# Performance work log

Measured on AMD Instinct MI355X. Metric: run time of the kernel, lower is better.

## Reference

```python
import jax, jax.numpy as jnp
import numpy as np

B, T, W, F, H = 4, 1024, 33, 512, 8
DK = F // H


def setup_inputs() -> dict:
    key = jax.random.key(0)
    ks = jax.random.split(key, 12)
    s = 1.0 / np.sqrt(F)
    return {
        "query": jax.random.normal(ks[0], (B, T, F), jnp.float32),
        "key": jax.random.normal(ks[1], (B, T, W, F), jnp.float32),
        "value": jax.random.normal(ks[2], (B, T, W, F), jnp.float32),
        "mask": jnp.ones((B, 1, T, W), jnp.int32),
        "Wq": jax.random.uniform(ks[3], (F, F), jnp.float32, -s, s),
        "bq": jax.random.uniform(ks[4], (F,), jnp.float32, -s, s),
        "Wk": jax.random.uniform(ks[5], (F, F), jnp.float32, -s, s),
        "bk": jax.random.uniform(ks[6], (F,), jnp.float32, -s, s),
        "Wv": jax.random.uniform(ks[7], (F, F), jnp.float32, -s, s),
        "bv": jax.random.uniform(ks[8], (F,), jnp.float32, -s, s),
        "Wo": jax.random.uniform(ks[9], (F, F), jnp.float32, -s, s),
        "bo": jax.random.uniform(ks[10], (F,), jnp.float32, -s, s),
    }


def reference(query, key, value, mask, Wq, bq, Wk, bk, Wv, bv, Wo, bo):
    b, t, w, f = key.shape
    # projections
    q = (query @ Wq + bq).reshape(b, t, H, DK)            # (B,T,H,Dk)
    k = (key @ Wk + bk).reshape(b, t, w, H, DK)           # (B,T,W,H,Dk)
    v = (value @ Wv + bv).reshape(b, t, w, H, DK)
    # windowed scores: each query attends to its own window of keys
    scores = jnp.einsum("bthd,btwhd->bhtw", q, k) / jnp.sqrt(jnp.asarray(DK, q.dtype))
    m = (mask == 0)                                       # (B,1,T,W), broadcasts over heads
    min_value = jnp.finfo(scores.dtype).min
    scores = jnp.where(m, min_value, scores)
    attn = jax.nn.softmax(scores, axis=-1)
    attn = jnp.where(m, 0.0, attn)                        # (B,H,T,W)
    x = jnp.einsum("bhtw,btwhd->bthd", attn, v).reshape(b, t, H * DK)
    return x @ Wo + bo
```

## Files before the change

kernel.cpp:

```cpp
#include <hip/hip_runtime.h>
#include <hip/hip_bf16.h>
#include <cstdint>

#define B_ 4
#define T_ 1024
#define W_ 33
#define F_ 512
#define H_ 8
#define DK_ 64

typedef __attribute__((ext_vector_type(8))) short short8;
typedef __attribute__((ext_vector_type(4))) float f32x4;

__device__ __forceinline__ float b2f(ushort u) {
  return __uint_as_float(((uint32_t)u) << 16);
}
__device__ __forceinline__ ushort f2b(float f) {
  union { __hip_bfloat16 b; ushort u; } cv;
  cv.b = __float2bfloat16(f);
  return cv.u;
}

__global__ void convert_w(const float* __restrict__ Wq, const float* __restrict__ Wk,
                          const float* __restrict__ Wv, const float* __restrict__ Wo,
                          ushort* __restrict__ out)
{
  int which = blockIdx.y;
  const float* src = (which == 0) ? Wq : (which == 1) ? Wk : (which == 2) ? Wv : Wo;
  ushort* dst = out + (size_t)which * 262144;
  int idx = blockIdx.x * 256 + threadIdx.x;
  int e = idx & 7;
  int l = (idx >> 3) & 63;
  float v;
  if (which == 1) {
    int kc  = (idx >> 9) & 1;
    int ntf = (idx >> 10) & 31;
    int h   = idx >> 15;
    v = src[(size_t)(ntf * 16 + (l & 15)) * 512 + h * 64 + kc * 32 + ((l >> 4) << 3) + e];
  } else {
    int kc = (idx >> 9) & 15;
    int nt = idx >> 13;
    int k = kc * 32 + ((l >> 4) << 3) + e;
    int n = (nt << 4) + (l & 15);
    v = src[(size_t)k * 512 + n];
  }
  dst[idx] = f2b(v);
}

template<bool A_F32, bool OUT_F32>
__global__ __launch_bounds__(256, 2)
void gemm_pipe(const void* __restrict__ Ap, const ushort* __restrict__ Bf,
               const float* __restrict__ bias, void* __restrict__ Cp, float scale)
{
  __shared__ ushort lA[3][128 * 64];

  const int tid  = threadIdx.x;
  const int lane = tid & 63;
  const int wid  = tid >> 6;
  const int wr   = wid >> 1, wc = wid & 1;
  const int lrow = lane & 15;
  const int lk8  = (lane >> 4) * 8;

  int nwg  = gridDim.x;
  int xcd  = blockIdx.x & 7;
  int slot = blockIdx.x >> 3;
  int q8   = nwg >> 3, r8 = nwg & 7;
  int base = (xcd < r8) ? xcd * (q8 + 1) : r8 * (q8 + 1) + (xcd - r8) * q8;
  int L    = base + slot;
  int bm   = L >> 2;
  int bn   = L & 3;

  int lb_[4];
  size_t asrc_[4];
#pragma unroll
  for (int p = 0; p < 4; ++p) {
    int c   = p * 256 + tid;
    int row = c >> 3;
    int kc  = (c & 7) * 8;
    lb_[p]  = (row * 128 + kc * 2) ^ ((row & 7) << 4);
    asrc_[p] = (size_t)(bm * 128 + row) * 512 + kc;
  }

  const int ntb = bn * 8 + wc * 4;

  float4 P0a0[4], P0a1[4], P1a0[4], P1a1[4];
  short8 P0r[4], P1r[4];
  short8 Q0[8], Q1[8];

  auto issueA = [&](int ks, float4 (&d0)[4], float4 (&d1)[4], short8 (&dr)[4]) {
#pragma unroll
    for (int p = 0; p < 4; ++p) {
      if (A_F32) {
        const float* src = (const float*)Ap + asrc_[p] + ks * 64;
        d0[p] = *(const float4*)src;
        d1[p] = *(const float4*)(src + 4);
      } else {
        dr[p] = *(const short8*)((const ushort*)Ap + asrc_[p] + ks * 64);
      }
    }
  };
  auto lwriteA = [&](int buf, float4 (&d0)[4], float4 (&d1)[4], short8 (&dr)[4]) {
#pragma unroll
    for (int p = 0; p < 4; ++p) {
      short8 hv;
      if (A_F32) {
        hv[0] = (short)f2b(d0[p].x); hv[1] = (short)f2b(d0[p].y);
        hv[2] = (short)f2b(d0[p].z); hv[3] = (short)f2b(d0[p].w);
        hv[4] = (short)f2b(d1[p].x); hv[5] = (short)f2b(d1[p].y);
        hv[6] = (short)f2b(d1[p].z); hv[7] = (short)f2b(d1[p].w);
      } else {
        hv = dr[p];
      }
      *(short8*)((char*)lA[buf] + lb_[p]) = hv;
    }
  };
  auto loadB = [&](int ks, short8 (&dq)[8]) {
#pragma unroll
    for (int kk = 0; kk < 2; ++kk)
#pragma unroll
      for (int nf = 0; nf < 4; ++nf)
        dq[kk * 4 + nf] = *(const short8*)(Bf +
            (((size_t)(ntb + nf) * 16 + ks * 2 + kk) * 64 + lane) * 8);
  };

  f32x4 acc[4][4];
#pragma unroll
  for (int i = 0; i < 4; ++i)
#pragma unroll
    for (int j = 0; j < 4; ++j) acc[i][j] = {0.f, 0.f, 0.f, 0.f};

  auto computeStep = [&](int buf, short8 (&dq)[8]) {
#pragma unroll
    for (int kk = 0; kk < 2; ++kk) {
      short8 af[4];
#pragma unroll
      for (int mf = 0; mf < 4; ++mf) {
        int row = wr * 64 + mf * 16 + lrow;
        int off = (row * 128 + (kk * 32 + lk8) * 2) ^ ((row & 7) << 4);
        af[mf] = *(const short8*)((const char*)lA[buf] + off);
      }
#pragma unroll
      for (int mf = 0; mf < 4; ++mf)
#pragma unroll
        for (int nf = 0; nf < 4; ++nf)
          acc[mf][nf] = __builtin_amdgcn_mfma_f32_16x16x32_bf16(af[mf], dq[kk * 4 + nf], acc[mf][nf], 0, 0, 0);
    }
  };

  issueA(0, P0a0, P0a1, P0r);
  issueA(1, P1a0, P1a1, P1r);
  loadB(0, Q0);
  lwriteA(0, P0a0, P0a1, P0r);
  __syncthreads();

#define GSTEP(T, PWa0, PWa1, PWr, PIa0, PIa1, PIr, QW, QR)                    \
  {                                                                           \
    if ((T) + 1 < 8) lwriteA(((T) + 1) % 3, PWa0, PWa1, PWr);                 \
    if ((T) + 2 < 8) issueA((T) + 2, PIa0, PIa1, PIr);                        \
    if ((T) + 1 < 8) loadB((T) + 1, QW);                                      \
    computeStep((T) % 3, QR);                                                 \
    if ((T) < 7) __syncthreads();                                             \
  }

  GSTEP(0, P1a0, P1a1, P1r, P0a0, P0a1, P0r, Q1, Q0)
  GSTEP(1, P0a0, P0a1, P0r, P1a0, P1a1, P1r, Q0, Q1)
  GSTEP(2, P1a0, P1a1, P1r, P0a0, P0a1, P0r, Q1, Q0)
  GSTEP(3, P0a0, P0a1, P0r, P1a0, P1a1, P1r, Q0, Q1)
  GSTEP(4, P1a0, P1a1, P1r, P0a0, P0a1, P0r, Q1, Q0)
  GSTEP(5, P0a0, P0a1, P0r, P1a0, P1a1, P1r, Q0, Q1)
  GSTEP(6, P1a0, P1a1, P1r, P0a0, P0a1, P0r, Q1, Q0)
  GSTEP(7, P0a0, P0a1, P0r, P1a0, P1a1, P1r, Q0, Q1)
#undef GSTEP

  float bs[4];
#pragma unroll
  for (int nf = 0; nf < 4; ++nf)
    bs[nf] = bias[bn * 128 + wc * 64 + nf * 16 + lrow];

  const int r0 = (lane >> 4) * 4;
#pragma unroll
  for (int mf = 0; mf < 4; ++mf) {
#pragma unroll
    for (int nf = 0; nf < 4; ++nf) {
      int gcol = bn * 128 + wc * 64 + nf * 16 + lrow;
#pragma unroll
      for (int r = 0; r < 4; ++r) {
        int grow = bm * 128 + wr * 64 + mf * 16 + r0 + r;
        float val = (acc[mf][nf][r] + bs[nf]) * scale;
        if (OUT_F32) ((float*)Cp)[(size_t)grow * 512 + gcol] = val;
        else         ((ushort*)Cp)[(size_t)grow * 512 + gcol] = f2b(val);
      }
    }
  }
}

__global__ __launch_bounds__(256, 4)
void r_gemm(const ushort* __restrict__ q, const ushort* __restrict__ WkR,
            ushort* __restrict__ R)
{
  const int tid  = threadIdx.x;
  const int lane = tid & 63;
  const int wid  = tid >> 6;
  const int lr   = lane & 15;
  const int l8   = (lane >> 4) * 8;
  const int mg   = blockIdx.x >> 1;
  const int nh   = blockIdx.x & 1;
  const int h    = blockIdx.y;
  const int m0   = mg * 64;
  const int ntb  = nh * 16 + wid * 4;

  short8 af[2][4], bg[2][4];
#pragma unroll
  for (int ks = 0; ks < 2; ++ks)
#pragma unroll
    for (int mf = 0; mf < 4; ++mf)
      af[ks][mf] = *(const short8*)(q + (size_t)(m0 + mf * 16 + lr) * 512 + h * 64 + ks * 32 + l8);
#pragma unroll
  for (int ks = 0; ks < 2; ++ks)
#pragma unroll
    for (int nf = 0; nf < 4; ++nf)
      bg[ks][nf] = *(const short8*)(WkR + ((size_t)((h * 32 + ntb + nf) * 2 + ks) * 64 + lane) * 8);

  f32x4 acc[4][4];
#pragma unroll
  for (int i = 0; i < 4; ++i)
#pragma unroll
    for (int j = 0; j < 4; ++j) acc[i][j] = {0.f, 0.f, 0.f, 0.f};

#pragma unroll
  for (int ks = 0; ks < 2; ++ks)
#pragma unroll
    for (int mf = 0; mf < 4; ++mf)
#pragma unroll
      for (int nf = 0; nf < 4; ++nf)
        acc[mf][nf] = __builtin_amdgcn_mfma_f32_16x16x32_bf16(af[ks][mf], bg[ks][nf], acc[mf][nf], 0, 0, 0);

  const int rr = (lane >> 4) * 4;
#pragma unroll
  for (int mf = 0; mf < 4; ++mf)
#pragma unroll
    for (int nf = 0; nf < 4; ++nf) {
      int col = nh * 256 + wid * 64 + nf * 16 + lr;
#pragma unroll
      for (int r = 0; r < 4; ++r) {
        int row = m0 + mf * 16 + rr + r;
        R[((size_t)row * 8 + h) * 512 + col] = f2b(acc[mf][nf][r]);
      }
    }
}

__global__ __launch_bounds__(256, 4)
void attn_fused(const float* __restrict__ key, const float* __restrict__ value,
                const ushort* __restrict__ R, const int* __restrict__ mask,
                ushort* __restrict__ g, float* __restrict__ asum)
{
  __shared__ float la[W_][8];
  __shared__ float linv[8];

  const int tid  = threadIdx.x;
  const int lane = tid & 63;
  const int wv   = tid >> 6;
  const int bt   = blockIdx.x;

  int mreg = 0;
  if (lane < W_) mreg = mask[(size_t)bt * W_ + lane];
  unsigned long long mbits = __ballot(mreg != 0);

  const int h0 = wv * 2;
  float Rf[2][8];
  {
    const ushort* Rb = R + (size_t)bt * 4096 + lane * 8;
    short8 rv0 = *(const short8*)(Rb + (size_t)h0 * 512);
    short8 rv1 = *(const short8*)(Rb + (size_t)(h0 + 1) * 512);
#pragma unroll
    for (int j = 0; j < 8; ++j) {
      Rf[0][j] = b2f((ushort)rv0[j]);
      Rf[1][j] = b2f((ushort)rv1[j]);
    }
  }

  const float* kb = key + (size_t)bt * (W_ * 512) + lane * 8;
#pragma unroll 3
  for (int w = 0; w < W_; ++w) {
    float4 ka = *(const float4*)(kb + (size_t)w * 512);
    float4 kc = *(const float4*)(kb + (size_t)w * 512 + 4);
    float s0 = ka.x * Rf[0][0] + ka.y * Rf[0][1] + ka.z * Rf[0][2] + ka.w * Rf[0][3]
             + kc.x * Rf[0][4] + kc.y * Rf[0][5] + kc.z * Rf[0][6] + kc.w * Rf[0][7];
    float s1 = ka.x * Rf[1][0] + ka.y * Rf[1][1] + ka.z * Rf[1][2] + ka.w * Rf[1][3]
             + kc.x * Rf[1][4] + kc.y * Rf[1][5] + kc.z * Rf[1][6] + kc.w * Rf[1][7];
#pragma unroll
    for (int m = 1; m < 64; m <<= 1) {
      s0 += __shfl_xor(s0, m, 64);
      s1 += __shfl_xor(s1, m, 64);
    }
    float t = (lane == 0) ? s0 : s1;
    float e = ((mbits >> w) & 1ull) ? __expf(t) : 0.f;
    if (lane < 2) la[w][h0 + lane] = e;
  }
  __syncthreads();

  const float* vb = value + (size_t)bt * (W_ * 512) + tid * 2;
  float2 vA[8], vB[8];
#pragma unroll
  for (int i = 0; i < 8; ++i) vA[i] = *(const float2*)(vb + (size_t)i * 512);
#pragma unroll
  for (int i = 0; i < 8; ++i) vB[i] = *(const float2*)(vb + (size_t)(8 + i) * 512);

  const int hh = tid & 7;
  float ss = 0.f;
#pragma unroll
  for (int w = 0; w < W_; ++w) ss += la[w][hh];
  if (tid < H_) {
    linv[tid] = (mbits != 0ull) ? 1.f / ss : 0.f;
    asum[(size_t)bt * H_ + tid] = (mbits != 0ull) ? 1.f : 0.f;
  }

  float gg0[8], gg1[8];
#pragma unroll
  for (int h = 0; h < 8; ++h) { gg0[h] = 0.f; gg1[h] = 0.f; }

  auto consume = [&](float2 v, int w) {
    f32x4 a0 = *(const f32x4*)&la[w][0];
    f32x4 a1 = *(const f32x4*)&la[w][4];
    gg0[0] += a0[0] * v.x; gg1[0] += a0[0] * v.y;
    gg0[1] += a0[1] * v.x; gg1[1] += a0[1] * v.y;
    gg0[2] += a0[2] * v.x; gg1[2] += a0[2] * v.y;
    gg0[3] += a0[3] * v.x; gg1[3] += a0[3] * v.y;
    gg0[4] += a1[0] * v.x; gg1[4] += a1[0] * v.y;
    gg0[5] += a1[1] * v.x; gg1[5] += a1[1] * v.y;
    gg0[6] += a1[2] * v.x; gg1[6] += a1[2] * v.y;
    gg0[7] += a1[3] * v.x; gg1[7] += a1[3] * v.y;
  };

#pragma unroll
  for (int i = 0; i < 8; ++i) consume(vA[i], i);
#pragma unroll
  for (int i = 0; i < 8; ++i) vA[i] = *(const float2*)(vb + (size_t)(16 + i) * 512);
#pragma unroll
  for (int i = 0; i < 8; ++i) consume(vB[i], 8 + i);
#pragma unroll
  for (int i = 0; i < 8; ++i) vB[i] = *(const float2*)(vb + (size_t)(24 + i) * 512);
#pragma unroll
  for (int i = 0; i < 8; ++i) consume(vA[i], 16 + i);
  float2 vL = *(const float2*)(vb + (size_t)32 * 512);
#pragma unroll
  for (int i = 0; i < 8; ++i) consume(vB[i], 24 + i);
  consume(vL, 32);

  __syncthreads();

  f32x4 iv0 = *(const f32x4*)&linv[0];
  f32x4 iv1 = *(const f32x4*)&linv[4];
  ushort* gb = g + (size_t)bt * 4096 + tid * 2;
#pragma unroll
  for (int h = 0; h < 8; ++h) {
    float iv = (h < 4) ? iv0[h & 3] : iv1[h & 3];
    ushort2 pk;
    pk.x = f2b(gg0[h] * iv);
    pk.y = f2b(gg1[h] * iv);
    *(ushort2*)(gb + h * 512) = pk;
  }
}

__global__ __launch_bounds__(256, 2)
void x_proj(const ushort* __restrict__ g, const ushort* __restrict__ WtV,
            const float* __restrict__ bv, const float* __restrict__ asum,
            ushort* __restrict__ x)
{
  const int tid  = threadIdx.x;
  const int lane = tid & 63;
  const int wid  = tid >> 6;
  const int lr   = lane & 15;
  const int l8   = (lane >> 4) * 8;
  const int h    = blockIdx.y;
  const int m0   = blockIdx.x * 256 + wid * 64;
  const int ntb  = h * 4;

  f32x4 acc[4][4];
#pragma unroll
  for (int i = 0; i < 4; ++i)
#pragma unroll
    for (int j = 0; j < 4; ++j) acc[i][j] = {0.f, 0.f, 0.f, 0.f};

  short8 a0[4], a1[4], b0[4], b1[4];

  auto issue = [&](int ks, short8 (&A)[4], short8 (&Bq)[4]) {
#pragma unroll
    for (int mf = 0; mf < 4; ++mf)
      A[mf] = *(const short8*)(g + ((size_t)(m0 + mf * 16 + lr) * 8 + h) * 512 + ks * 32 + l8);
#pragma unroll
    for (int nf = 0; nf < 4; ++nf)
      Bq[nf] = *(const short8*)(WtV + ((size_t)((ntb + nf) * 16 + ks) * 64 + lane) * 8);
  };
  auto step = [&](short8 (&A)[4], short8 (&Bq)[4]) {
#pragma unroll
    for (int mf = 0; mf < 4; ++mf)
#pragma unroll
      for (int nf = 0; nf < 4; ++nf)
        acc[mf][nf] = __builtin_amdgcn_mfma_f32_16x16x32_bf16(A[mf], Bq[nf], acc[mf][nf], 0, 0, 0);
  };

  issue(0, a0, b0);
  issue(1, a1, b1);
#pragma unroll 1
  for (int ks = 0; ks < 16; ks += 2) {
    step(a0, b0);
    if (ks + 2 < 16) issue(ks + 2, a0, b0);
    step(a1, b1);
    if (ks + 3 < 16) issue(ks + 3, a1, b1);
  }

  float bvv[4];
#pragma unroll
  for (int nf = 0; nf < 4; ++nf)
    bvv[nf] = bv[h * 64 + nf * 16 + lr];

  const int rr = (lane >> 4) * 4;
#pragma unroll
  for (int mf = 0; mf < 4; ++mf)
#pragma unroll
    for (int nf = 0; nf < 4; ++nf) {
      int col = h * 64 + nf * 16 + lr;
#pragma unroll
      for (int r = 0; r < 4; ++r) {
        int row = m0 + mf * 16 + rr + r;
        float val = acc[mf][nf][r] + asum[(size_t)row * 8 + h] * bvv[nf];
        x[(size_t)row * 512 + col] = f2b(val);
      }
    }
}

extern "C" void kernel_launch(void* const* d_in, const int* in_sizes, int n_in,
                              void* d_out, int out_size, void* d_ws, size_t ws_size,
                              hipStream_t stream)
{
  const float* query = (const float*)d_in[0];
  const float* key   = (const float*)d_in[1];
  const float* value = (const float*)d_in[2];
  const int*   mask  = (const int*)d_in[3];
  const float* Wq    = (const float*)d_in[4];
  const float* bq    = (const float*)d_in[5];
  const float* Wk    = (const float*)d_in[6];
  const float* bk    = (const float*)d_in[7];
  const float* Wv    = (const float*)d_in[8];
  const float* bv    = (const float*)d_in[9];
  const float* Wo    = (const float*)d_in[10];
  const float* bo    = (const float*)d_in[11];
  (void)bk;

  char* ws = (char*)d_ws;
  ushort* Wt   = (ushort*)ws;
  ushort* WtQ  = Wt;
  ushort* WkR  = Wt + 262144;
  ushort* WtV  = Wt + 524288;
  ushort* WtO  = Wt + 786432;
  ushort* qws  = (ushort*)(ws + (size_t)2  * 1024 * 1024);
  ushort* Rws  = (ushort*)(ws + (size_t)6  * 1024 * 1024);
  ushort* gws  = (ushort*)(ws + (size_t)38 * 1024 * 1024);
  float*  asum = (float*) (ws + (size_t)70 * 1024 * 1024);
  ushort* xws  = (ushort*)(ws + (size_t)71 * 1024 * 1024);

  convert_w<<<dim3(1024, 4), 256, 0, stream>>>(Wq, Wk, Wv, Wo, Wt);

  gemm_pipe<true, false><<<dim3(128, 1), 256, 0, stream>>>(query, WtQ, bq, qws, 0.125f);

  r_gemm<<<dim3(128, 8), 256, 0, stream>>>(qws, WkR, Rws);

  attn_fused<<<dim3(B_ * T_, 1), 256, 0, stream>>>(key, value, Rws, mask, gws, asum);

  x_proj<<<dim3(16, 8), 256, 0, stream>>>(gws, WtV, bv, asum, xws);

  gemm_pipe<false, true><<<dim3(128, 1), 256, 0, stream>>>(xws, WtO, bo, d_out, 1.0f);
}
```

Baseline: 221.0 us.

## Split fused attention into separate scores and PV kernels for higher occupancy

```diff
diff --git a/kernel.cpp b/kernel.cpp
--- a/kernel.cpp
+++ b/kernel.cpp
@@ -249,13 +249,12 @@
     }
 }
 
-__global__ __launch_bounds__(256, 4)
-void attn_fused(const float* __restrict__ key, const float* __restrict__ value,
-                const ushort* __restrict__ R, const int* __restrict__ mask,
-                ushort* __restrict__ g, float* __restrict__ asum)
+__global__ __launch_bounds__(256, 6)
+void attn_scores(const float* __restrict__ key, const ushort* __restrict__ R,
+                 const int* __restrict__ mask, float* __restrict__ probs,
+                 float* __restrict__ asum)
 {
   __shared__ float la[W_][8];
-  __shared__ float linv[8];
 
   const int tid  = threadIdx.x;
   const int lane = tid & 63;
@@ -299,29 +298,43 @@
   }
   __syncthreads();
 
-  const float* vb = value + (size_t)bt * (W_ * 512) + tid * 2;
-  float2 vA[8], vB[8];
-#pragma unroll
-  for (int i = 0; i < 8; ++i) vA[i] = *(const float2*)(vb + (size_t)i * 512);
-#pragma unroll
-  for (int i = 0; i < 8; ++i) vB[i] = *(const float2*)(vb + (size_t)(8 + i) * 512);
-
   const int hh = tid & 7;
   float ss = 0.f;
 #pragma unroll
   for (int w = 0; w < W_; ++w) ss += la[w][hh];
-  if (tid < H_) {
-    linv[tid] = (mbits != 0ull) ? 1.f / ss : 0.f;
+  float inv = (mbits != 0ull) ? 1.f / ss : 0.f;
+
+  for (int t = tid; t < H_ * W_; t += 256) {
+    int w = t >> 3;
+    probs[(size_t)bt * 264 + t] = la[w][hh] * inv;
+  }
+  if (tid < H_)
     asum[(size_t)bt * H_ + tid] = (mbits != 0ull) ? 1.f : 0.f;
-  }
-
+}
+
+__global__ __launch_bounds__(256, 8)
+void attn_pv(const float* __restrict__ value, const float* __restrict__ probs,
+             ushort* __restrict__ g)
+{
+  __shared__ float lp[W_ * 8];
+
+  const int tid = threadIdx.x;
+  const int bt  = blockIdx.x;
+
+  for (int c = tid; c < W_ * 8; c += 256)
+    lp[c] = probs[(size_t)bt * 264 + c];
+  __syncthreads();
+
+  const float* vb = value + (size_t)bt * (W_ * 512) + tid * 2;
   float gg0[8], gg1[8];
 #pragma unroll
   for (int h = 0; h < 8; ++h) { gg0[h] = 0.f; gg1[h] = 0.f; }
 
-  auto consume = [&](float2 v, int w) {
-    f32x4 a0 = *(const f32x4*)&la[w][0];
-    f32x4 a1 = *(const f32x4*)&la[w][4];
+#pragma unroll
+  for (int w = 0; w < W_; ++w) {
+    float2 v = *(const float2*)(vb + (size_t)w * 512);
+    f32x4 a0 = *(const f32x4*)&lp[w * 8];
+    f32x4 a1 = *(const f32x4*)&lp[w * 8 + 4];
     gg0[0] += a0[0] * v.x; gg1[0] += a0[0] * v.y;
     gg0[1] += a0[1] * v.x; gg1[1] += a0[1] * v.y;
     gg0[2] += a0[2] * v.x; gg1[2] += a0[2] * v.y;
@@ -330,34 +343,14 @@
     gg0[5] += a1[1] * v.x; gg1[5] += a1[1] * v.y;
     gg0[6] += a1[2] * v.x; gg1[6] += a1[2] * v.y;
     gg0[7] += a1[3] * v.x; gg1[7] += a1[3] * v.y;
-  };
-
-#pragma unroll
-  for (int i = 0; i < 8; ++i) consume(vA[i], i);
-#pragma unroll
-  for (int i = 0; i < 8; ++i) vA[i] = *(const float2*)(vb + (size_t)(16 + i) * 512);
-#pragma unroll
-  for (int i = 0; i < 8; ++i) consume(vB[i], 8 + i);
-#pragma unroll
-  for (int i = 0; i < 8; ++i) vB[i] = *(const float2*)(vb + (size_t)(24 + i) * 512);
-#pragma unroll
-  for (int i = 0; i < 8; ++i) consume(vA[i], 16 + i);
-  float2 vL = *(const float2*)(vb + (size_t)32 * 512);
-#pragma unroll
-  for (int i = 0; i < 8; ++i) consume(vB[i], 24 + i);
-  consume(vL, 32);
-
-  __syncthreads();
-
-  f32x4 iv0 = *(const f32x4*)&linv[0];
-  f32x4 iv1 = *(const f32x4*)&linv[4];
+  }
+
   ushort* gb = g + (size_t)bt * 4096 + tid * 2;
 #pragma unroll
   for (int h = 0; h < 8; ++h) {
-    float iv = (h < 4) ? iv0[h & 3] : iv1[h & 3];
     ushort2 pk;
-    pk.x = f2b(gg0[h] * iv);
-    pk.y = f2b(gg1[h] * iv);
+    pk.x = f2b(gg0[h]);
+    pk.y = f2b(gg1[h]);
     *(ushort2*)(gb + h * 512) = pk;
   }
 }
@@ -449,16 +442,17 @@
   (void)bk;
 
   char* ws = (char*)d_ws;
-  ushort* Wt   = (ushort*)ws;
-  ushort* WtQ  = Wt;
-  ushort* WkR  = Wt + 262144;
-  ushort* WtV  = Wt + 524288;
-  ushort* WtO  = Wt + 786432;
-  ushort* qws  = (ushort*)(ws + (size_t)2  * 1024 * 1024);
-  ushort* Rws  = (ushort*)(ws + (size_t)6  * 1024 * 1024);
-  ushort* gws  = (ushort*)(ws + (size_t)38 * 1024 * 1024);
-  float*  asum = (float*) (ws + (size_t)70 * 1024 * 1024);
-  ushort* xws  = (ushort*)(ws + (size_t)71 * 1024 * 1024);
+  ushort* Wt    = (ushort*)ws;
+  ushort* WtQ   = Wt;
+  ushort* WkR   = Wt + 262144;
+  ushort* WtV   = Wt + 524288;
+  ushort* WtO   = Wt + 786432;
+  ushort* qws   = (ushort*)(ws + (size_t)2  * 1024 * 1024);
+  ushort* Rws   = (ushort*)(ws + (size_t)6  * 1024 * 1024);
+  ushort* gws   = (ushort*)(ws + (size_t)38 * 1024 * 1024);
+  float*  asum  = (float*) (ws + (size_t)70 * 1024 * 1024);
+  float*  probs = (float*) (ws + (size_t)70 * 1024 * 1024 + 256 * 1024);
+  ushort* xws   = qws;
 
   convert_w<<<dim3(1024, 4), 256, 0, stream>>>(Wq, Wk, Wv, Wo, Wt);
 
@@ -466,7 +460,9 @@
 
   r_gemm<<<dim3(128, 8), 256, 0, stream>>>(qws, WkR, Rws);
 
-  attn_fused<<<dim3(B_ * T_, 1), 256, 0, stream>>>(key, value, Rws, mask, gws, asum);
+  attn_scores<<<dim3(B_ * T_, 1), 256, 0, stream>>>(key, Rws, mask, probs, asum);
+
+  attn_pv<<<dim3(B_ * T_, 1), 256, 0, stream>>>(value, probs, gws);
 
   x_proj<<<dim3(16, 8), 256, 0, stream>>>(gws, WtV, bv, asum, xws);
 
```

Measured after the change: 211.5 us. 1.04x faster.
